# Kernel optimization log

Hardware: AMD Instinct MI355X
Metric: run time of the kernel (lower is better)

## Reference

```python
import jax, jax.numpy as jnp
import numpy as np

X_DIM = [128, 256, 512]
IMG_H, IMG_W = 105, 105
T = 1000
DT, TAU = 0.01, 1.0
K = 32
P_MIN = 1e-16


def setup_inputs() -> dict:
    key = jax.random.key(0)
    ks = jax.random.split(key, 12)

    def rn(k, shape, scale=1.0):
        return jax.random.normal(k, shape, jnp.float32) * scale

    # binary image with one 'on' pixel -> initial pen position via argwhere
    data = jnp.zeros((IMG_H, IMG_W), bool).at[52, 52].set(True)
    return {
        'data': data,
        'z1': jax.random.uniform(ks[0], (K,), jnp.float32),          # top-layer alphas
        'z2': rn(ks[1], (X_DIM[0],)),                                 # top-layer init state
        'gamma': jax.random.uniform(ks[2], (3,), jnp.float32, 0.3, 0.7),
        'pen_log_var': jnp.array(2.0, jnp.float32),
        'W_a0': rn(ks[3], (K, X_DIM[0]), X_DIM[0] ** -0.5),
        'W_a1': rn(ks[4], (K, X_DIM[1]), X_DIM[1] ** -0.5),
        'b_a0': jnp.zeros((K,), jnp.float32),
        'b_a1': jnp.zeros((K,), jnp.float32),
        'W_u0': rn(ks[5], (X_DIM[1], X_DIM[0]), X_DIM[0] ** -0.5),
        'W_u1': rn(ks[6], (X_DIM[2], X_DIM[1]), X_DIM[1] ** -0.5),
        'W_p': rn(ks[7], (3, X_DIM[2]), X_DIM[2] ** -0.5),
        'b_p': jnp.zeros((3,), jnp.float32),
        # attractor dynamics matrices, scaled for stable Euler integration
        'A0': rn(ks[8], (K, X_DIM[0], X_DIM[0]), 0.5 * X_DIM[0] ** -0.5),
        'A1': rn(ks[9], (K, X_DIM[1], X_DIM[1]), 0.5 * X_DIM[1] ** -0.5),
        'A2': rn(ks[10], (K, X_DIM[2], X_DIM[2]), 0.5 * X_DIM[2] ** -0.5),
    }


def _decode(data, z1, z2, gamma, pen_log_var, W_a0, W_a1, b_a0, b_a1,
            W_u0, W_u1, W_p, b_p, A0, A1, A2):
    grid_x = jnp.linspace(0.5, IMG_W - 0.5, IMG_W)
    grid_y = jnp.linspace(0.5, IMG_H - 0.5, IMG_H)
    img_dims = jnp.array([IMG_H, IMG_W], jnp.float32)
    # stabilise_variance: lower-bound the variance
    log_var = jnp.log(jnp.exp(pen_log_var) + P_MIN)
    inv_var = jnp.exp(-log_var)

    def step(carry, z1_t):
        x, pen_xy = carry
        alphas = [z1_t,
                  jax.nn.softmax(W_a0 @ x[0] + b_a0, axis=0),
                  jax.nn.softmax(W_a1 @ x[1] + b_a1, axis=0)]
        u = [jnp.zeros_like(x[0]), W_u0 @ x[0], W_u1 @ x[1]]

        def upd(A, g, xl, al, ul):
            aAx = jnp.einsum('k,kij,j->i', al, A, xl)  # alpha-weighted attractor drive
            return xl + ((1 - g) * aAx - g * xl + ul) * (DT / TAU)

        x_new = [upd(A0, gamma[0], x[0], alphas[0], u[0]),
                 upd(A1, gamma[1], x[1], alphas[1], u[1]),
                 upd(A2, gamma[2], x[2], alphas[2], u[2])]
        pen_actions = W_p @ x_new[2] + b_p
        d_xy = pen_actions[:2]
        pen_down_log_p = jax.nn.log_sigmoid(pen_actions[2])
        # per-pixel Bernoulli parameter: separable Gaussian kernel on the grid
        ll_y = -0.5 * (pen_xy[0] - grid_y) ** 2 * inv_var
        ll_x = -0.5 * (pen_xy[1] - grid_x) ** 2 * inv_var
        p_xy = jnp.exp(ll_y[:, None] + ll_x[None, :] + pen_down_log_p)
        p_xy = p_xy * (1 - 2 * P_MIN) + P_MIN  # stabilise_cross_entropy
        # pen position update with sigmoid squashing to the image
        pen = pen_xy + d_xy
        pen = jax.nn.sigmoid((pen - img_dims / 2) * 4 / img_dims) * img_dims
        return (x_new, pen), (alphas, u, x_new, pen, p_xy, pen_down_log_p)

    x0 = [z2, jnp.zeros((X_DIM[1],), jnp.float32), jnp.zeros((X_DIM[2],), jnp.float32)]
    pen_xy0 = jnp.argwhere(data, size=1)[0].astype(jnp.float32)
    inputs = jnp.broadcast_to(z1[None, :], (T, K))
    _, (alphas, u, x, pen_xy, p_xy_t, pen_down_log_p) = jax.lax.scan(step, (x0, pen_xy0), inputs)
    return (*alphas, *u, *x, pen_xy, p_xy_t, pen_down_log_p)


def reference(data, z1, z2, gamma, pen_log_var, W_a0, W_a1, b_a0, b_a1,
              W_u0, W_u1, W_p, b_p, A0, A1, A2):
    return _decode(data, z1, z2, gamma, pen_log_var, W_a0, W_a1, b_a0, b_a1,
                   W_u0, W_u1, W_p, b_p, A0, A1, A2)
```

## Files before the change

kernel.cpp:

```cpp
#include <hip/hip_runtime.h>
#include <math.h>

#define T_STEPS 1000
#define KK 32
#define D0 128
#define D1 256
#define D2 512
#define IMGH 105
#define IMGW 105
#define NPIX (IMGH*IMGW)
#define DTTAU 0.01f

#define NB 256
#define NT 512

#define OFF_M0   0
#define OFF_X0S  16384
#define OFF_X1S  16640
#define OFF_X2S  17152
#define OFF_S2T  18176
#define OFF_PA   530176
#define OFF_PXYP 533176
#define OFF_PENS 536176
#define OFF_CTR  536192

#define OA0  0
#define OA1  32000
#define OA2  64000
#define OU0  96000
#define OU1  224000
#define OU2  480000
#define OX0  992000
#define OX1  1120000
#define OX2  1376000
#define OPEN 1888000
#define OPXY 1890000
#define OPDLP 12915000

#define DOT4(a,b) ((a).x*(b).x + (a).y*(b).y + (a).z*(b).z + (a).w*(b).w)

__device__ __forceinline__ float waveReduceSum(float v) {
    for (int m = 32; m >= 1; m >>= 1) v += __shfl_xor(v, m, 64);
    return v;
}

__global__ __launch_bounds__(256) void setup_kernel(
    const void* __restrict__ dataRaw, const float* __restrict__ z2,
    float* __restrict__ ws)
{
    if (blockIdx.x != 0) return;
    int tid = threadIdx.x;

    if (tid < D0) (ws + OFF_X0S)[tid] = z2[tid];
    if (tid < D1) (ws + OFF_X1S)[tid] = 0.f;
    for (int i = tid; i < D2; i += 256) (ws + OFF_X2S)[i] = 0.f;
    if (tid < 128) ((int*)(ws + OFF_CTR))[tid] = 0;

    __shared__ int sMin;
    if (tid == 0) sMin = 0x7fffffff;
    __syncthreads();
    const unsigned char* db = (const unsigned char*)dataRaw;
    for (int i = tid; i < NPIX; i += 256) if (db[i]) atomicMin(&sMin, i);
    __syncthreads();
    if (sMin == 0x7fffffff) {
        const int* di = (const int*)dataRaw;
        for (int i = tid; i < NPIX; i += 256) if (di[i] != 0) atomicMin(&sMin, i);
    }
    __syncthreads();
    if (tid == 0) {
        int idx = (sMin == 0x7fffffff) ? 0 : sMin;
        (ws + OFF_PENS)[0] = (float)(idx / IMGW);
        (ws + OFF_PENS)[1] = (float)(idx % IMGW);
    }
}

__global__ __launch_bounds__(256) void m0_kernel(
    const float* __restrict__ z1, const float* __restrict__ A0, float* __restrict__ ws)
{
    int idx = blockIdx.x * 256 + threadIdx.x;
    if (idx < D0 * D0) {
        float s = 0.f;
        for (int k = 0; k < KK; k++) s += z1[k] * A0[(size_t)k * D0 * D0 + idx];
        ws[OFF_M0 + idx] = s;
    }
}

__global__ __launch_bounds__(256) void fill_kernel(const float* __restrict__ z1, float* __restrict__ out)
{
    size_t gid = (size_t)blockIdx.x * blockDim.x + threadIdx.x;
    size_t nthr = (size_t)gridDim.x * blockDim.x;
    for (size_t i = gid; i < 32000; i += nthr) out[OA0 + i] = z1[i & 31];
    for (size_t i = gid; i < 128000; i += nthr) out[OU0 + i] = 0.f;
}

__global__ __launch_bounds__(NT, 2) void persist_kernel(
    const float* __restrict__ A1, const float* __restrict__ A2,
    const float* __restrict__ Wu0, const float* __restrict__ Wu1,
    const float* __restrict__ Wa0, const float* __restrict__ Wa1,
    const float* __restrict__ ba0, const float* __restrict__ ba1,
    const float* __restrict__ gam,
    float* __restrict__ ws, float* __restrict__ out)
{
    const int b = blockIdx.x;
    const int tid = threadIdx.x;
    const int lane = tid & 63;
    const int w = tid >> 6;
    const int k = tid >> 4;
    const int c = tid & 15;

    float4 a2r0[8], a2r1[8], a1r[4];
    {
        const float4* p0 = (const float4*)(A2 + ((size_t)k * D2 + 2 * b) * D2 + c * 32);
        const float4* p1 = (const float4*)(A2 + ((size_t)k * D2 + 2 * b + 1) * D2 + c * 32);
        #pragma unroll
        for (int jj = 0; jj < 8; ++jj) { a2r0[jj] = p0[jj]; a2r1[jj] = p1[jj]; }
        const float4* p2 = (const float4*)(A1 + ((size_t)k * D1 + b) * D1 + c * 16);
        #pragma unroll
        for (int jj = 0; jj < 4; ++jj) a1r[jj] = p2[jj];
    }
    const float g0 = gam[0], g1 = gam[1], g2 = gam[2];

    __shared__ __align__(16) float x0s[D0];
    __shared__ __align__(16) float x1s[16 * 20];
    __shared__ __align__(16) float x2s[16 * 36];
    __shared__ float pre[64];
    __shared__ float red2a[KK], red2b[KK], red1[KK];
    __shared__ float uS[3];

    float* X0S = ws + OFF_X0S;
    float* X1S = ws + OFF_X1S;
    float* X2S = ws + OFF_X2S;
    int* ctr = (int*)(ws + OFF_CTR);

    #pragma unroll 1
    for (int t = 0; t < T_STEPS; ++t) {
        const int p = t & 1;

        if (tid < D0)
            x0s[tid] = __hip_atomic_load(&X0S[p * D0 + tid], __ATOMIC_RELAXED, __HIP_MEMORY_SCOPE_AGENT);
        if (tid < D1)
            x1s[(tid >> 4) * 20 + (tid & 15)] =
                __hip_atomic_load(&X1S[p * D1 + tid], __ATOMIC_RELAXED, __HIP_MEMORY_SCOPE_AGENT);
        x2s[(tid >> 5) * 36 + (tid & 31)] =
            __hip_atomic_load(&X2S[p * D2 + tid], __ATOMIC_RELAXED, __HIP_MEMORY_SCOPE_AGENT);
        __syncthreads();

        {
            float s = 0.f;
            const float4* wr = (const float4*)(Wa1 + (size_t)k * D1 + c * 16);
            const float4* xc = (const float4*)(x1s + c * 20);
            #pragma unroll
            for (int jj = 0; jj < 4; ++jj) { float4 a = wr[jj], x = xc[jj]; s += DOT4(a, x); }
            s += __shfl_xor(s, 1, 64); s += __shfl_xor(s, 2, 64);
            s += __shfl_xor(s, 4, 64); s += __shfl_xor(s, 8, 64);
            if (c == 0) pre[k] = s + ba1[k];

            float s1 = 0.f;
            const float4* wr1 = (const float4*)(Wa0 + (size_t)k * D0 + c * 8);
            const float4* xc1 = (const float4*)(x0s + c * 8);
            #pragma unroll
            for (int jj = 0; jj < 2; ++jj) { float4 a = wr1[jj], x = xc1[jj]; s1 += DOT4(a, x); }
            s1 += __shfl_xor(s1, 1, 64); s1 += __shfl_xor(s1, 2, 64);
            s1 += __shfl_xor(s1, 4, 64); s1 += __shfl_xor(s1, 8, 64);
            if (c == 0) pre[32 + k] = s1 + ba0[k];

            const float4* x24 = (const float4*)x2s;
            float sa = 0.f, sb = 0.f;
            #pragma unroll
            for (int jj = 0; jj < 8; ++jj) {
                float4 x = x24[c * 9 + jj];
                sa += DOT4(a2r0[jj], x);
                sb += DOT4(a2r1[jj], x);
            }
            sa += __shfl_xor(sa, 1, 64); sa += __shfl_xor(sa, 2, 64);
            sa += __shfl_xor(sa, 4, 64); sa += __shfl_xor(sa, 8, 64);
            sb += __shfl_xor(sb, 1, 64); sb += __shfl_xor(sb, 2, 64);
            sb += __shfl_xor(sb, 4, 64); sb += __shfl_xor(sb, 8, 64);
            const float4* x14 = (const float4*)x1s;
            float sc = 0.f;
            #pragma unroll
            for (int jj = 0; jj < 4; ++jj) {
                float4 x = x14[c * 5 + jj];
                sc += DOT4(a1r[jj], x);
            }
            sc += __shfl_xor(sc, 1, 64); sc += __shfl_xor(sc, 2, 64);
            sc += __shfl_xor(sc, 4, 64); sc += __shfl_xor(sc, 8, 64);
            if (c == 0) { red2a[k] = sa; red2b[k] = sb; red1[k] = sc; }
        }
        if (w == 4 || w == 5) {
            int eg = 2 * b + (w - 4);
            const float4* wr = (const float4*)(Wu1 + (size_t)eg * D1);
            const float4* x4 = (const float4*)x1s;
            float4 a = wr[lane];
            float4 x = x4[(lane >> 2) * 5 + (lane & 3)];
            float s = DOT4(a, x);
            s = waveReduceSum(s);
            if (lane == 0) { uS[w - 4] = s; out[OU2 + (size_t)t * D2 + eg] = s; }
        } else if (w == 6) {
            float s = 0.f;
            if (lane < 32) {
                const float4* wr = (const float4*)(Wu0 + (size_t)b * D0);
                const float4* x4 = (const float4*)x0s;
                float4 a = wr[lane], x = x4[lane];
                s = DOT4(a, x);
            }
            s = waveReduceSum(s);
            if (lane == 0) { uS[2] = s; out[OU1 + (size_t)t * D1 + b] = s; }
        } else if (w == 7 && b < D0) {
            float s = 0.f;
            if (lane < 32) {
                const float4* mr = (const float4*)(ws + OFF_M0 + (size_t)b * D0);
                const float4* x4 = (const float4*)x0s;
                float4 a = mr[lane], x = x4[lane];
                s = DOT4(a, x);
            }
            s = waveReduceSum(s);
            if (lane == 0) {
                float xo = x0s[b];
                float xn = xo + ((1.f - g0) * s - g0 * xo) * DTTAU;
                __hip_atomic_store(&X0S[(p ^ 1) * D0 + b], xn, __ATOMIC_RELAXED, __HIP_MEMORY_SCOPE_AGENT);
                out[OX0 + (size_t)t * D0 + b] = xn;
            }
        }
        __syncthreads();

        if (w == 0) {
            float pv = pre[lane];
            float m = pv;
            m = fmaxf(m, __shfl_xor(m, 16, 64)); m = fmaxf(m, __shfl_xor(m, 8, 64));
            m = fmaxf(m, __shfl_xor(m, 4, 64));  m = fmaxf(m, __shfl_xor(m, 2, 64));
            m = fmaxf(m, __shfl_xor(m, 1, 64));
            float e = expf(pv - m);
            float ss = e;
            ss += __shfl_xor(ss, 16, 64); ss += __shfl_xor(ss, 8, 64);
            ss += __shfl_xor(ss, 4, 64);  ss += __shfl_xor(ss, 2, 64); ss += __shfl_xor(ss, 1, 64);
            float al = e / ss;
            if (b == 0) {
                if (lane < 32) out[OA2 + (size_t)t * KK + lane] = al;
                else           out[OA1 + (size_t)t * KK + (lane - 32)] = al;
            }
            float r1 = (lane < 32) ? red2a[lane] : red1[lane - 32];
            float r2 = (lane < 32) ? red2b[lane] : 0.f;
            float v1 = al * r1, v2 = al * r2;
            v1 += __shfl_xor(v1, 16, 64); v1 += __shfl_xor(v1, 8, 64);
            v1 += __shfl_xor(v1, 4, 64);  v1 += __shfl_xor(v1, 2, 64); v1 += __shfl_xor(v1, 1, 64);
            v2 += __shfl_xor(v2, 16, 64); v2 += __shfl_xor(v2, 8, 64);
            v2 += __shfl_xor(v2, 4, 64);  v2 += __shfl_xor(v2, 2, 64); v2 += __shfl_xor(v2, 1, 64);
            if (lane == 0) {
                int eg = 2 * b;
                float xo0 = x2s[(eg >> 5) * 36 + (eg & 31)];
                float xn0 = xo0 + ((1.f - g2) * v1 - g2 * xo0 + uS[0]) * DTTAU;
                __hip_atomic_store(&X2S[(p ^ 1) * D2 + eg], xn0, __ATOMIC_RELAXED, __HIP_MEMORY_SCOPE_AGENT);
                out[OX2 + (size_t)t * D2 + eg] = xn0;
                ws[OFF_S2T + (size_t)t * D2 + eg] = xn0;
                int eh = eg + 1;
                float xo1 = x2s[(eh >> 5) * 36 + (eh & 31)];
                float xn1 = xo1 + ((1.f - g2) * v2 - g2 * xo1 + uS[1]) * DTTAU;
                __hip_atomic_store(&X2S[(p ^ 1) * D2 + eh], xn1, __ATOMIC_RELAXED, __HIP_MEMORY_SCOPE_AGENT);
                out[OX2 + (size_t)t * D2 + eh] = xn1;
                ws[OFF_S2T + (size_t)t * D2 + eh] = xn1;
            }
            if (lane == 32) {
                float xo = x1s[(b >> 4) * 20 + (b & 15)];
                float xn = xo + ((1.f - g1) * v1 - g1 * xo + uS[2]) * DTTAU;
                __hip_atomic_store(&X1S[(p ^ 1) * D1 + b], xn, __ATOMIC_RELAXED, __HIP_MEMORY_SCOPE_AGENT);
                out[OX1 + (size_t)t * D1 + b] = xn;
            }
            if (t < T_STEPS - 1) {
                asm volatile("s_waitcnt vmcnt(0)" ::: "memory");
                if (lane == 0)
                    __hip_atomic_fetch_add(&ctr[(b & 7) * 16], 1, __ATOMIC_RELAXED, __HIP_MEMORY_SCOPE_AGENT);
                const int target = NB * (t + 1);
                if (lane < 8) {
                    int s;
                    do {
                        int v = __hip_atomic_load(&ctr[lane * 16], __ATOMIC_RELAXED, __HIP_MEMORY_SCOPE_AGENT);
                        s = v;
                        s += __shfl_xor(s, 1, 64);
                        s += __shfl_xor(s, 2, 64);
                        s += __shfl_xor(s, 4, 64);
                        if (s < target) __builtin_amdgcn_s_sleep(1);
                    } while (s < target);
                }
            }
        }
        __syncthreads();
    }
}

__global__ __launch_bounds__(192) void pa_kernel(
    const float* __restrict__ Wp, const float* __restrict__ bp, float* __restrict__ ws)
{
    int t = blockIdx.x;
    int w = threadIdx.x >> 6, lane = threadIdx.x & 63;
    const float4* x2 = (const float4*)(ws + OFF_S2T + (size_t)t * D2);
    const float4* wr = (const float4*)(Wp + (size_t)w * D2);
    float p = 0.f;
    #pragma unroll
    for (int it = 0; it < 2; ++it) {
        float4 a = wr[lane + 64 * it], x = x2[lane + 64 * it];
        p += DOT4(a, x);
    }
    p = waveReduceSum(p);
    if (lane == 0) ws[OFF_PA + (size_t)t * 3 + w] = p + bp[w];
}

__global__ void chain_kernel(float* __restrict__ ws, float* __restrict__ out)
{
    if (blockIdx.x != 0 || threadIdx.x != 0) return;
    float py = ws[OFF_PENS], px = ws[OFF_PENS + 1];
    for (int t = 0; t < T_STEPS; ++t) {
        float dy = ws[OFF_PA + t * 3], dx = ws[OFF_PA + t * 3 + 1], z = ws[OFF_PA + t * 3 + 2];
        float pdlp = fminf(z, 0.f) - log1pf(expf(-fabsf(z)));
        ws[OFF_PXYP + t * 3] = py; ws[OFF_PXYP + t * 3 + 1] = px; ws[OFF_PXYP + t * 3 + 2] = pdlp;
        float ny = py + dy, nx = px + dx;
        ny = 105.f / (1.f + expf(-(ny - 52.5f) * (4.f / 105.f)));
        nx = 105.f / (1.f + expf(-(nx - 52.5f) * (4.f / 105.f)));
        py = ny; px = nx;
        out[OPEN + (size_t)t * 2] = py;
        out[OPEN + (size_t)t * 2 + 1] = px;
        out[OPDLP + t] = pdlp;
    }
}

__global__ __launch_bounds__(256) void pxy_kernel(
    const float* __restrict__ plv, const float* __restrict__ ws, float* __restrict__ out)
{
    int t = blockIdx.x;
    const float* pxyp = ws + OFF_PXYP + (size_t)t * 3;
    float py = pxyp[0], px = pxyp[1], pdlp = pxyp[2];
    float inv_var = 1.0f / (expf(plv[0]) + 1e-16f);
    for (int p = threadIdx.x; p < NPIX; p += 256) {
        int i = p / IMGW, j = p % IMGW;
        float ddy = py - ((float)i + 0.5f);
        float ddx = px - ((float)j + 0.5f);
        float v = expf(-0.5f * inv_var * (ddy * ddy + ddx * ddx) + pdlp);
        out[OPXY + (size_t)t * NPIX + p] = v + 1e-16f;
    }
}

extern "C" void kernel_launch(void* const* d_in, const int* in_sizes, int n_in,
                              void* d_out, int out_size, void* d_ws, size_t ws_size,
                              hipStream_t stream)
{
    const void*  data = d_in[0];
    const float* z1  = (const float*)d_in[1];
    const float* z2  = (const float*)d_in[2];
    const float* gam = (const float*)d_in[3];
    const float* plv = (const float*)d_in[4];
    const float* Wa0 = (const float*)d_in[5];
    const float* Wa1 = (const float*)d_in[6];
    const float* ba0 = (const float*)d_in[7];
    const float* ba1 = (const float*)d_in[8];
    const float* Wu0 = (const float*)d_in[9];
    const float* Wu1 = (const float*)d_in[10];
    const float* Wp  = (const float*)d_in[11];
    const float* bp  = (const float*)d_in[12];
    const float* A0  = (const float*)d_in[13];
    const float* A1  = (const float*)d_in[14];
    const float* A2  = (const float*)d_in[15];
    float* out = (float*)d_out;
    float* ws  = (float*)d_ws;

    hipLaunchKernelGGL(setup_kernel, dim3(1), dim3(256), 0, stream, data, z2, ws);
    hipLaunchKernelGGL(m0_kernel, dim3(64), dim3(256), 0, stream, z1, A0, ws);
    hipLaunchKernelGGL(fill_kernel, dim3(128), dim3(256), 0, stream, z1, out);
    hipLaunchKernelGGL(persist_kernel, dim3(NB), dim3(NT), 0, stream,
                       A1, A2, Wu0, Wu1, Wa0, Wa1, ba0, ba1, gam, ws, out);
    hipLaunchKernelGGL(pa_kernel, dim3(T_STEPS), dim3(192), 0, stream, Wp, bp, ws);
    hipLaunchKernelGGL(chain_kernel, dim3(1), dim3(64), 0, stream, ws, out);
    hipLaunchKernelGGL(pxy_kernel, dim3(T_STEPS), dim3(256), 0, stream, plv, ws, out);
}
```

Before: 5.926 ms.

## Replace global barrier with stamped value flags and fuse pen projection into persistent loop

Each state element is now stored as a 64-bit (timestamp, value) pair, so blocks spin on the specific values they need instead of on a grid-wide counter barrier. This removes the atomic counter and the sleep-based all-block wait on every step. The Wp projection and the pen-down log-probability are computed inside the persistent kernel one step late, which drops the separate pa_kernel and the full x2 history write. The cost is 64-bit polling loads over every element and extra work in wave 1 of each block; correctness depends on the stamp ordering with relaxed atomics.

```diff
diff --git a/kernel.cpp b/kernel.cpp
--- a/kernel.cpp
+++ b/kernel.cpp
@@ -14,15 +14,16 @@
 #define NB 256
 #define NT 512
 
+typedef unsigned long long ull;
+
 #define OFF_M0   0
-#define OFF_X0S  16384
-#define OFF_X1S  16640
-#define OFF_X2S  17152
-#define OFF_S2T  18176
-#define OFF_PA   530176
-#define OFF_PXYP 533176
-#define OFF_PENS 536176
-#define OFF_CTR  536192
+#define OFF_PX0  16384
+#define OFF_PX1  16896
+#define OFF_PX2  17920
+#define OFF_S2T  19968
+#define OFF_PA   531968
+#define OFF_PXYP 534968
+#define OFF_PENS 537968
 
 #define OA0  0
 #define OA1  32000
@@ -43,6 +44,9 @@
     for (int m = 32; m >= 1; m >>= 1) v += __shfl_xor(v, m, 64);
     return v;
 }
+__device__ __forceinline__ ull packPair(float v, unsigned stamp) {
+    return ((ull)stamp << 32) | (ull)__float_as_uint(v);
+}
 
 __global__ __launch_bounds__(256) void setup_kernel(
     const void* __restrict__ dataRaw, const float* __restrict__ z2,
@@ -50,11 +54,14 @@
 {
     if (blockIdx.x != 0) return;
     int tid = threadIdx.x;
-
-    if (tid < D0) (ws + OFF_X0S)[tid] = z2[tid];
-    if (tid < D1) (ws + OFF_X1S)[tid] = 0.f;
-    for (int i = tid; i < D2; i += 256) (ws + OFF_X2S)[i] = 0.f;
-    if (tid < 128) ((int*)(ws + OFF_CTR))[tid] = 0;
+    ull* PX0 = (ull*)(ws + OFF_PX0);
+    ull* PX1 = (ull*)(ws + OFF_PX1);
+    ull* PX2 = (ull*)(ws + OFF_PX2);
+    const ull INVALID = 0xFFFFFFFF00000000ULL;
+
+    if (tid < D0) { PX0[tid] = packPair(z2[tid], 0); PX0[D0 + tid] = INVALID; }
+    if (tid < D1) { PX1[tid] = packPair(0.f, 0);     PX1[D1 + tid] = INVALID; }
+    for (int i = tid; i < D2; i += 256) { PX2[i] = packPair(0.f, 0); PX2[D2 + i] = INVALID; }
 
     __shared__ int sMin;
     if (tid == 0) sMin = 0x7fffffff;
@@ -98,6 +105,7 @@
     const float* __restrict__ Wu0, const float* __restrict__ Wu1,
     const float* __restrict__ Wa0, const float* __restrict__ Wa1,
     const float* __restrict__ ba0, const float* __restrict__ ba1,
+    const float* __restrict__ Wp, const float* __restrict__ bp,
     const float* __restrict__ gam,
     float* __restrict__ ws, float* __restrict__ out)
 {
@@ -127,22 +135,37 @@
     __shared__ float red2a[KK], red2b[KK], red1[KK];
     __shared__ float uS[3];
 
-    float* X0S = ws + OFF_X0S;
-    float* X1S = ws + OFF_X1S;
-    float* X2S = ws + OFF_X2S;
-    int* ctr = (int*)(ws + OFF_CTR);
+    ull* PX0 = (ull*)(ws + OFF_PX0);
+    ull* PX1 = (ull*)(ws + OFF_PX1);
+    ull* PX2 = (ull*)(ws + OFF_PX2);
+
+    const int hasB1 = (tid < 256);
+    const int hasB0 = (tid >= 256 && tid < 384);
 
     #pragma unroll 1
     for (int t = 0; t < T_STEPS; ++t) {
         const int p = t & 1;
-
-        if (tid < D0)
-            x0s[tid] = __hip_atomic_load(&X0S[p * D0 + tid], __ATOMIC_RELAXED, __HIP_MEMORY_SCOPE_AGENT);
-        if (tid < D1)
-            x1s[(tid >> 4) * 20 + (tid & 15)] =
-                __hip_atomic_load(&X1S[p * D1 + tid], __ATOMIC_RELAXED, __HIP_MEMORY_SCOPE_AGENT);
-        x2s[(tid >> 5) * 36 + (tid & 31)] =
-            __hip_atomic_load(&X2S[p * D2 + tid], __ATOMIC_RELAXED, __HIP_MEMORY_SCOPE_AGENT);
+        const unsigned want = (unsigned)t;
+
+        {
+            ull pa_ = 0, pb_ = 0;
+            bool okA = false, okB = !(hasB1 || hasB0);
+            ull* srcB = hasB1 ? &PX1[p * D1 + tid]
+                              : (hasB0 ? &PX0[p * D0 + (tid - 256)] : (ull*)0);
+            do {
+                if (!okA) {
+                    pa_ = __hip_atomic_load(&PX2[p * D2 + tid], __ATOMIC_RELAXED, __HIP_MEMORY_SCOPE_AGENT);
+                    okA = ((unsigned)(pa_ >> 32) == want);
+                }
+                if (!okB) {
+                    pb_ = __hip_atomic_load(srcB, __ATOMIC_RELAXED, __HIP_MEMORY_SCOPE_AGENT);
+                    okB = ((unsigned)(pb_ >> 32) == want);
+                }
+            } while (!(okA && okB));
+            x2s[(tid >> 5) * 36 + (tid & 31)] = __uint_as_float((unsigned)pa_);
+            if (hasB1) x1s[(tid >> 4) * 20 + (tid & 15)] = __uint_as_float((unsigned)pb_);
+            else if (hasB0) x0s[tid - 256] = __uint_as_float((unsigned)pb_);
+        }
         __syncthreads();
 
         {
@@ -187,7 +210,31 @@
             sc += __shfl_xor(sc, 4, 64); sc += __shfl_xor(sc, 8, 64);
             if (c == 0) { red2a[k] = sa; red2b[k] = sb; red1[k] = sc; }
         }
-        if (w == 4 || w == 5) {
+        if (w == 1 && t > 0) {
+            const float4* x24 = (const float4*)x2s;
+            #pragma unroll
+            for (int r = 0; r < 3; ++r) {
+                const float4* wr = (const float4*)(Wp + (size_t)r * D2);
+                float s = 0.f;
+                #pragma unroll
+                for (int it = 0; it < 2; ++it) {
+                    int e4 = lane + 64 * it;
+                    float4 x = x24[(e4 >> 3) * 9 + (e4 & 7)];
+                    float4 a = wr[e4];
+                    s += DOT4(a, x);
+                }
+                s = waveReduceSum(s);
+                if (lane == 0) {
+                    if (r < 2) ws[OFF_PA + (size_t)(t - 1) * 3 + r] = s + bp[r];
+                    else {
+                        float z = s + bp[2];
+                        float pdlp = fminf(z, 0.f) - log1pf(expf(-fabsf(z)));
+                        ws[OFF_PA + (size_t)(t - 1) * 3 + 2] = pdlp;
+                        out[OPDLP + (t - 1)] = pdlp;
+                    }
+                }
+            }
+        } else if (w == 4 || w == 5) {
             int eg = 2 * b + (w - 4);
             const float4* wr = (const float4*)(Wu1 + (size_t)eg * D1);
             const float4* x4 = (const float4*)x1s;
@@ -218,7 +265,8 @@
             if (lane == 0) {
                 float xo = x0s[b];
                 float xn = xo + ((1.f - g0) * s - g0 * xo) * DTTAU;
-                __hip_atomic_store(&X0S[(p ^ 1) * D0 + b], xn, __ATOMIC_RELAXED, __HIP_MEMORY_SCOPE_AGENT);
+                __hip_atomic_store(&PX0[(p ^ 1) * D0 + b], packPair(xn, (unsigned)(t + 1)),
+                                   __ATOMIC_RELAXED, __HIP_MEMORY_SCOPE_AGENT);
                 out[OX0 + (size_t)t * D0 + b] = xn;
             }
         }
@@ -250,68 +298,63 @@
                 int eg = 2 * b;
                 float xo0 = x2s[(eg >> 5) * 36 + (eg & 31)];
                 float xn0 = xo0 + ((1.f - g2) * v1 - g2 * xo0 + uS[0]) * DTTAU;
-                __hip_atomic_store(&X2S[(p ^ 1) * D2 + eg], xn0, __ATOMIC_RELAXED, __HIP_MEMORY_SCOPE_AGENT);
+                __hip_atomic_store(&PX2[(p ^ 1) * D2 + eg], packPair(xn0, (unsigned)(t + 1)),
+                                   __ATOMIC_RELAXED, __HIP_MEMORY_SCOPE_AGENT);
                 out[OX2 + (size_t)t * D2 + eg] = xn0;
-                ws[OFF_S2T + (size_t)t * D2 + eg] = xn0;
                 int eh = eg + 1;
                 float xo1 = x2s[(eh >> 5) * 36 + (eh & 31)];
                 float xn1 = xo1 + ((1.f - g2) * v2 - g2 * xo1 + uS[1]) * DTTAU;
-                __hip_atomic_store(&X2S[(p ^ 1) * D2 + eh], xn1, __ATOMIC_RELAXED, __HIP_MEMORY_SCOPE_AGENT);
+                __hip_atomic_store(&PX2[(p ^ 1) * D2 + eh], packPair(xn1, (unsigned)(t + 1)),
+                                   __ATOMIC_RELAXED, __HIP_MEMORY_SCOPE_AGENT);
                 out[OX2 + (size_t)t * D2 + eh] = xn1;
-                ws[OFF_S2T + (size_t)t * D2 + eh] = xn1;
+                if (t == T_STEPS - 1) {
+                    ws[OFF_S2T + (size_t)t * D2 + eg] = xn0;
+                    ws[OFF_S2T + (size_t)t * D2 + eh] = xn1;
+                }
             }
             if (lane == 32) {
                 float xo = x1s[(b >> 4) * 20 + (b & 15)];
                 float xn = xo + ((1.f - g1) * v1 - g1 * xo + uS[2]) * DTTAU;
-                __hip_atomic_store(&X1S[(p ^ 1) * D1 + b], xn, __ATOMIC_RELAXED, __HIP_MEMORY_SCOPE_AGENT);
+                __hip_atomic_store(&PX1[(p ^ 1) * D1 + b], packPair(xn, (unsigned)(t + 1)),
+                                   __ATOMIC_RELAXED, __HIP_MEMORY_SCOPE_AGENT);
                 out[OX1 + (size_t)t * D1 + b] = xn;
             }
-            if (t < T_STEPS - 1) {
-                asm volatile("s_waitcnt vmcnt(0)" ::: "memory");
-                if (lane == 0)
-                    __hip_atomic_fetch_add(&ctr[(b & 7) * 16], 1, __ATOMIC_RELAXED, __HIP_MEMORY_SCOPE_AGENT);
-                const int target = NB * (t + 1);
-                if (lane < 8) {
-                    int s;
-                    do {
-                        int v = __hip_atomic_load(&ctr[lane * 16], __ATOMIC_RELAXED, __HIP_MEMORY_SCOPE_AGENT);
-                        s = v;
-                        s += __shfl_xor(s, 1, 64);
-                        s += __shfl_xor(s, 2, 64);
-                        s += __shfl_xor(s, 4, 64);
-                        if (s < target) __builtin_amdgcn_s_sleep(1);
-                    } while (s < target);
-                }
-            }
         }
         __syncthreads();
     }
 }
 
-__global__ __launch_bounds__(192) void pa_kernel(
-    const float* __restrict__ Wp, const float* __restrict__ bp, float* __restrict__ ws)
-{
-    int t = blockIdx.x;
-    int w = threadIdx.x >> 6, lane = threadIdx.x & 63;
-    const float4* x2 = (const float4*)(ws + OFF_S2T + (size_t)t * D2);
-    const float4* wr = (const float4*)(Wp + (size_t)w * D2);
-    float p = 0.f;
-    #pragma unroll
-    for (int it = 0; it < 2; ++it) {
-        float4 a = wr[lane + 64 * it], x = x2[lane + 64 * it];
-        p += DOT4(a, x);
-    }
-    p = waveReduceSum(p);
-    if (lane == 0) ws[OFF_PA + (size_t)t * 3 + w] = p + bp[w];
-}
-
-__global__ void chain_kernel(float* __restrict__ ws, float* __restrict__ out)
-{
-    if (blockIdx.x != 0 || threadIdx.x != 0) return;
+__global__ __launch_bounds__(192) void chain_kernel(
+    const float* __restrict__ Wp, const float* __restrict__ bp,
+    float* __restrict__ ws, float* __restrict__ out)
+{
+    int tid = threadIdx.x;
+    int w = tid >> 6, lane = tid & 63;
+    {
+        const float4* x2 = (const float4*)(ws + OFF_S2T + (size_t)(T_STEPS - 1) * D2);
+        const float4* wr = (const float4*)(Wp + (size_t)w * D2);
+        float p = 0.f;
+        #pragma unroll
+        for (int it = 0; it < 2; ++it) {
+            float4 a = wr[lane + 64 * it], x = x2[lane + 64 * it];
+            p += DOT4(a, x);
+        }
+        p = waveReduceSum(p);
+        if (lane == 0) {
+            if (w < 2) ws[OFF_PA + (size_t)(T_STEPS - 1) * 3 + w] = p + bp[w];
+            else {
+                float z = p + bp[2];
+                float pdlp = fminf(z, 0.f) - log1pf(expf(-fabsf(z)));
+                ws[OFF_PA + (size_t)(T_STEPS - 1) * 3 + 2] = pdlp;
+                out[OPDLP + (T_STEPS - 1)] = pdlp;
+            }
+        }
+    }
+    __syncthreads();
+    if (tid != 0) return;
     float py = ws[OFF_PENS], px = ws[OFF_PENS + 1];
     for (int t = 0; t < T_STEPS; ++t) {
-        float dy = ws[OFF_PA + t * 3], dx = ws[OFF_PA + t * 3 + 1], z = ws[OFF_PA + t * 3 + 2];
-        float pdlp = fminf(z, 0.f) - log1pf(expf(-fabsf(z)));
+        float dy = ws[OFF_PA + t * 3], dx = ws[OFF_PA + t * 3 + 1], pdlp = ws[OFF_PA + t * 3 + 2];
         ws[OFF_PXYP + t * 3] = py; ws[OFF_PXYP + t * 3 + 1] = px; ws[OFF_PXYP + t * 3 + 2] = pdlp;
         float ny = py + dy, nx = px + dx;
         ny = 105.f / (1.f + expf(-(ny - 52.5f) * (4.f / 105.f)));
@@ -319,7 +362,6 @@
         py = ny; px = nx;
         out[OPEN + (size_t)t * 2] = py;
         out[OPEN + (size_t)t * 2 + 1] = px;
-        out[OPDLP + t] = pdlp;
     }
 }
 
@@ -366,8 +408,7 @@
     hipLaunchKernelGGL(m0_kernel, dim3(64), dim3(256), 0, stream, z1, A0, ws);
     hipLaunchKernelGGL(fill_kernel, dim3(128), dim3(256), 0, stream, z1, out);
     hipLaunchKernelGGL(persist_kernel, dim3(NB), dim3(NT), 0, stream,
-                       A1, A2, Wu0, Wu1, Wa0, Wa1, ba0, ba1, gam, ws, out);
-    hipLaunchKernelGGL(pa_kernel, dim3(T_STEPS), dim3(192), 0, stream, Wp, bp, ws);
-    hipLaunchKernelGGL(chain_kernel, dim3(1), dim3(64), 0, stream, ws, out);
+                       A1, A2, Wu0, Wu1, Wa0, Wa1, ba0, ba1, Wp, bp, gam, ws, out);
+    hipLaunchKernelGGL(chain_kernel, dim3(1), dim3(192), 0, stream, Wp, bp, ws, out);
     hipLaunchKernelGGL(pxy_kernel, dim3(T_STEPS), dim3(256), 0, stream, plv, ws, out);
 }
```

Result: slower. 6.066 ms (+2.4%).

## Fuse pen-action projection into persistent kernel and defer output stores past barrier

Applied to the files above, without the earlier changes.

Each persistent block computes the W_p projection of the previous step's x2 state (read from its local copy) using a wave that was otherwise idle, replacing the separate pa_kernel launch and the per-step x2 workspace writes. The final step's projection moves into a widened chain_kernel, and pen-down log-probabilities are computed once per step inside the persistent kernel. Global output stores for alphas and states are moved after the grid barrier so the barrier's vmcnt wait no longer covers them. In exchange every block redundantly does the small projection each step, which adds work to the critical per-step loop.

```diff
diff --git a/kernel.cpp b/kernel.cpp
--- a/kernel.cpp
+++ b/kernel.cpp
@@ -98,6 +98,7 @@
     const float* __restrict__ Wu0, const float* __restrict__ Wu1,
     const float* __restrict__ Wa0, const float* __restrict__ Wa1,
     const float* __restrict__ ba0, const float* __restrict__ ba1,
+    const float* __restrict__ Wp, const float* __restrict__ bp,
     const float* __restrict__ gam,
     float* __restrict__ ws, float* __restrict__ out)
 {
@@ -187,7 +188,31 @@
             sc += __shfl_xor(sc, 4, 64); sc += __shfl_xor(sc, 8, 64);
             if (c == 0) { red2a[k] = sa; red2b[k] = sb; red1[k] = sc; }
         }
-        if (w == 4 || w == 5) {
+        if (w == 1 && t > 0) {
+            const float4* x24 = (const float4*)x2s;
+            #pragma unroll
+            for (int r = 0; r < 3; ++r) {
+                const float4* wr = (const float4*)(Wp + (size_t)r * D2);
+                float s = 0.f;
+                #pragma unroll
+                for (int it = 0; it < 2; ++it) {
+                    int e4 = lane + 64 * it;
+                    float4 x = x24[(e4 >> 3) * 9 + (e4 & 7)];
+                    float4 a = wr[e4];
+                    s += DOT4(a, x);
+                }
+                s = waveReduceSum(s);
+                if (lane == 0) {
+                    if (r < 2) ws[OFF_PA + (size_t)(t - 1) * 3 + r] = s + bp[r];
+                    else {
+                        float z = s + bp[2];
+                        float pdlp = fminf(z, 0.f) - log1pf(expf(-fabsf(z)));
+                        ws[OFF_PA + (size_t)(t - 1) * 3 + 2] = pdlp;
+                        out[OPDLP + (t - 1)] = pdlp;
+                    }
+                }
+            }
+        } else if (w == 4 || w == 5) {
             int eg = 2 * b + (w - 4);
             const float4* wr = (const float4*)(Wu1 + (size_t)eg * D1);
             const float4* x4 = (const float4*)x1s;
@@ -235,10 +260,6 @@
             ss += __shfl_xor(ss, 16, 64); ss += __shfl_xor(ss, 8, 64);
             ss += __shfl_xor(ss, 4, 64);  ss += __shfl_xor(ss, 2, 64); ss += __shfl_xor(ss, 1, 64);
             float al = e / ss;
-            if (b == 0) {
-                if (lane < 32) out[OA2 + (size_t)t * KK + lane] = al;
-                else           out[OA1 + (size_t)t * KK + (lane - 32)] = al;
-            }
             float r1 = (lane < 32) ? red2a[lane] : red1[lane - 32];
             float r2 = (lane < 32) ? red2b[lane] : 0.f;
             float v1 = al * r1, v2 = al * r2;
@@ -246,25 +267,22 @@
             v1 += __shfl_xor(v1, 4, 64);  v1 += __shfl_xor(v1, 2, 64); v1 += __shfl_xor(v1, 1, 64);
             v2 += __shfl_xor(v2, 16, 64); v2 += __shfl_xor(v2, 8, 64);
             v2 += __shfl_xor(v2, 4, 64);  v2 += __shfl_xor(v2, 2, 64); v2 += __shfl_xor(v2, 1, 64);
+
+            float xn0 = 0.f, xn1 = 0.f, xnl1 = 0.f;
             if (lane == 0) {
                 int eg = 2 * b;
                 float xo0 = x2s[(eg >> 5) * 36 + (eg & 31)];
-                float xn0 = xo0 + ((1.f - g2) * v1 - g2 * xo0 + uS[0]) * DTTAU;
+                xn0 = xo0 + ((1.f - g2) * v1 - g2 * xo0 + uS[0]) * DTTAU;
                 __hip_atomic_store(&X2S[(p ^ 1) * D2 + eg], xn0, __ATOMIC_RELAXED, __HIP_MEMORY_SCOPE_AGENT);
-                out[OX2 + (size_t)t * D2 + eg] = xn0;
-                ws[OFF_S2T + (size_t)t * D2 + eg] = xn0;
                 int eh = eg + 1;
                 float xo1 = x2s[(eh >> 5) * 36 + (eh & 31)];
-                float xn1 = xo1 + ((1.f - g2) * v2 - g2 * xo1 + uS[1]) * DTTAU;
+                xn1 = xo1 + ((1.f - g2) * v2 - g2 * xo1 + uS[1]) * DTTAU;
                 __hip_atomic_store(&X2S[(p ^ 1) * D2 + eh], xn1, __ATOMIC_RELAXED, __HIP_MEMORY_SCOPE_AGENT);
-                out[OX2 + (size_t)t * D2 + eh] = xn1;
-                ws[OFF_S2T + (size_t)t * D2 + eh] = xn1;
             }
             if (lane == 32) {
                 float xo = x1s[(b >> 4) * 20 + (b & 15)];
-                float xn = xo + ((1.f - g1) * v1 - g1 * xo + uS[2]) * DTTAU;
-                __hip_atomic_store(&X1S[(p ^ 1) * D1 + b], xn, __ATOMIC_RELAXED, __HIP_MEMORY_SCOPE_AGENT);
-                out[OX1 + (size_t)t * D1 + b] = xn;
+                xnl1 = xo + ((1.f - g1) * v1 - g1 * xo + uS[2]) * DTTAU;
+                __hip_atomic_store(&X1S[(p ^ 1) * D1 + b], xnl1, __ATOMIC_RELAXED, __HIP_MEMORY_SCOPE_AGENT);
             }
             if (t < T_STEPS - 1) {
                 asm volatile("s_waitcnt vmcnt(0)" ::: "memory");
@@ -283,35 +301,56 @@
                     } while (s < target);
                 }
             }
+            if (b == 0) {
+                if (lane < 32) out[OA2 + (size_t)t * KK + lane] = al;
+                else           out[OA1 + (size_t)t * KK + (lane - 32)] = al;
+            }
+            if (lane == 0) {
+                int eg = 2 * b;
+                out[OX2 + (size_t)t * D2 + eg] = xn0;
+                out[OX2 + (size_t)t * D2 + eg + 1] = xn1;
+                if (t == T_STEPS - 1) {
+                    ws[OFF_S2T + (size_t)t * D2 + eg] = xn0;
+                    ws[OFF_S2T + (size_t)t * D2 + eg + 1] = xn1;
+                }
+            }
+            if (lane == 32) out[OX1 + (size_t)t * D1 + b] = xnl1;
         }
         __syncthreads();
     }
 }
 
-__global__ __launch_bounds__(192) void pa_kernel(
-    const float* __restrict__ Wp, const float* __restrict__ bp, float* __restrict__ ws)
-{
-    int t = blockIdx.x;
-    int w = threadIdx.x >> 6, lane = threadIdx.x & 63;
-    const float4* x2 = (const float4*)(ws + OFF_S2T + (size_t)t * D2);
-    const float4* wr = (const float4*)(Wp + (size_t)w * D2);
-    float p = 0.f;
-    #pragma unroll
-    for (int it = 0; it < 2; ++it) {
-        float4 a = wr[lane + 64 * it], x = x2[lane + 64 * it];
-        p += DOT4(a, x);
-    }
-    p = waveReduceSum(p);
-    if (lane == 0) ws[OFF_PA + (size_t)t * 3 + w] = p + bp[w];
-}
-
-__global__ void chain_kernel(float* __restrict__ ws, float* __restrict__ out)
-{
-    if (blockIdx.x != 0 || threadIdx.x != 0) return;
+__global__ __launch_bounds__(192) void chain_kernel(
+    const float* __restrict__ Wp, const float* __restrict__ bp,
+    float* __restrict__ ws, float* __restrict__ out)
+{
+    int tid = threadIdx.x;
+    int w = tid >> 6, lane = tid & 63;
+    {
+        const float4* x2 = (const float4*)(ws + OFF_S2T + (size_t)(T_STEPS - 1) * D2);
+        const float4* wr = (const float4*)(Wp + (size_t)w * D2);
+        float p = 0.f;
+        #pragma unroll
+        for (int it = 0; it < 2; ++it) {
+            float4 a = wr[lane + 64 * it], x = x2[lane + 64 * it];
+            p += DOT4(a, x);
+        }
+        p = waveReduceSum(p);
+        if (lane == 0) {
+            if (w < 2) ws[OFF_PA + (size_t)(T_STEPS - 1) * 3 + w] = p + bp[w];
+            else {
+                float z = p + bp[2];
+                float pdlp = fminf(z, 0.f) - log1pf(expf(-fabsf(z)));
+                ws[OFF_PA + (size_t)(T_STEPS - 1) * 3 + 2] = pdlp;
+                out[OPDLP + (T_STEPS - 1)] = pdlp;
+            }
+        }
+    }
+    __syncthreads();
+    if (tid != 0) return;
     float py = ws[OFF_PENS], px = ws[OFF_PENS + 1];
     for (int t = 0; t < T_STEPS; ++t) {
-        float dy = ws[OFF_PA + t * 3], dx = ws[OFF_PA + t * 3 + 1], z = ws[OFF_PA + t * 3 + 2];
-        float pdlp = fminf(z, 0.f) - log1pf(expf(-fabsf(z)));
+        float dy = ws[OFF_PA + t * 3], dx = ws[OFF_PA + t * 3 + 1], pdlp = ws[OFF_PA + t * 3 + 2];
         ws[OFF_PXYP + t * 3] = py; ws[OFF_PXYP + t * 3 + 1] = px; ws[OFF_PXYP + t * 3 + 2] = pdlp;
         float ny = py + dy, nx = px + dx;
         ny = 105.f / (1.f + expf(-(ny - 52.5f) * (4.f / 105.f)));
@@ -319,7 +358,6 @@
         py = ny; px = nx;
         out[OPEN + (size_t)t * 2] = py;
         out[OPEN + (size_t)t * 2 + 1] = px;
-        out[OPDLP + t] = pdlp;
     }
 }
 
@@ -366,8 +404,7 @@
     hipLaunchKernelGGL(m0_kernel, dim3(64), dim3(256), 0, stream, z1, A0, ws);
     hipLaunchKernelGGL(fill_kernel, dim3(128), dim3(256), 0, stream, z1, out);
     hipLaunchKernelGGL(persist_kernel, dim3(NB), dim3(NT), 0, stream,
-                       A1, A2, Wu0, Wu1, Wa0, Wa1, ba0, ba1, gam, ws, out);
-    hipLaunchKernelGGL(pa_kernel, dim3(T_STEPS), dim3(192), 0, stream, Wp, bp, ws);
-    hipLaunchKernelGGL(chain_kernel, dim3(1), dim3(64), 0, stream, ws, out);
+                       A1, A2, Wu0, Wu1, Wa0, Wa1, ba0, ba1, Wp, bp, gam, ws, out);
+    hipLaunchKernelGGL(chain_kernel, dim3(1), dim3(192), 0, stream, Wp, bp, ws, out);
     hipLaunchKernelGGL(pxy_kernel, dim3(T_STEPS), dim3(256), 0, stream, plv, ws, out);
 }
```

Result: slower. 6.620 ms (+11.7%).
